# Performance work log

Measured on AMD Instinct MI355X. Metric: run time of the kernel, lower is better.

## Reference

```python
import jax, jax.numpy as jnp
import numpy as np

SHAPES = [(16, 32, 32), (8, 16, 16), (4, 8, 8), (2, 4, 4)]  # (D,H,W) per level
B, DM, M, LV, P, NL, DFF = 2, 256, 8, 4, 4, 2, 1024
DH = DM // M
LEN = sum(d * h * w for d, h, w in SHAPES)
EPS = 1e-5


def setup_inputs() -> dict:
    key = jax.random.key(0)
    ks = iter(jax.random.split(key, 64))
    inp = {}
    for i, (d_, h_, w_) in enumerate(SHAPES):
        inp[f"src{i}"] = jax.random.normal(next(ks), (B, DM, d_, h_, w_), jnp.float32)
        inp[f"pos{i}"] = jax.random.normal(next(ks), (B, DM, d_, h_, w_), jnp.float32) * 0.1
    inp["level_embed"] = jax.random.normal(next(ks), (LV, DM), jnp.float32)
    s = 1.0 / np.sqrt(DM)
    inp["W_off"] = jax.random.normal(next(ks), (NL, DM, M * LV * P * 3), jnp.float32) * 0.02
    inp["b_off"] = jax.random.normal(next(ks), (NL, M * LV * P * 3), jnp.float32) * 0.2
    inp["W_attn"] = jax.random.normal(next(ks), (NL, DM, M * LV * P), jnp.float32) * s
    inp["b_attn"] = jnp.zeros((NL, M * LV * P), jnp.float32)
    inp["W_val"] = jax.random.normal(next(ks), (NL, DM, DM), jnp.float32) * s
    inp["b_val"] = jnp.zeros((NL, DM), jnp.float32)
    inp["W_out"] = jax.random.normal(next(ks), (NL, DM, DM), jnp.float32) * s
    inp["b_out"] = jnp.zeros((NL, DM), jnp.float32)
    inp["ln1_g"] = jnp.ones((NL, DM), jnp.float32)
    inp["ln1_b"] = jnp.zeros((NL, DM), jnp.float32)
    inp["W_ff1"] = jax.random.normal(next(ks), (NL, DM, DFF), jnp.float32) * s
    inp["b_ff1"] = jnp.zeros((NL, DFF), jnp.float32)
    inp["W_ff2"] = jax.random.normal(next(ks), (NL, DFF, DM), jnp.float32) * (1.0 / np.sqrt(DFF))
    inp["b_ff2"] = jnp.zeros((NL, DM), jnp.float32)
    inp["ln2_g"] = jnp.ones((NL, DM), jnp.float32)
    inp["ln2_b"] = jnp.zeros((NL, DM), jnp.float32)
    return inp


def _layer_norm(x, g, b):
    mu = jnp.mean(x, -1, keepdims=True)
    var = jnp.mean(jnp.square(x - mu), -1, keepdims=True)
    return (x - mu) * jax.lax.rsqrt(var + EPS) * g + b


def _trilinear_sample(value_bm, loc, D_, H_, W_):
    """value_bm: [B, M, D*H*W, DH]; loc: [B, Lq, M, P, 3] normalized in [0,1].
    grid_sample(align_corners=False, padding=zeros) semantics: comp0->W, comp1->H, comp2->D."""
    x = loc[..., 0] * W_ - 0.5
    y = loc[..., 1] * H_ - 0.5
    z = loc[..., 2] * D_ - 0.5
    x0, y0, z0 = jnp.floor(x), jnp.floor(y), jnp.floor(z)
    fx, fy, fz = x - x0, y - y0, z - z0
    x0i, y0i, z0i = x0.astype(jnp.int32), y0.astype(jnp.int32), z0.astype(jnp.int32)
    Bq, Lq = loc.shape[0], loc.shape[1]
    out = jnp.zeros((Bq, M, Lq * P, DH), value_bm.dtype)
    for dz in (0, 1):
        for dy in (0, 1):
            for dx in (0, 1):
                xi, yi, zi = x0i + dx, y0i + dy, z0i + dz
                w = ((fx if dx else 1.0 - fx) * (fy if dy else 1.0 - fy) * (fz if dz else 1.0 - fz))
                valid = ((xi >= 0) & (xi < W_) & (yi >= 0) & (yi < H_) & (zi >= 0) & (zi < D_))
                idx = (jnp.clip(zi, 0, D_ - 1) * H_ + jnp.clip(yi, 0, H_ - 1)) * W_ + jnp.clip(xi, 0, W_ - 1)
                idx_bm = jnp.transpose(idx, (0, 2, 1, 3)).reshape(Bq, M, Lq * P)  # [B,M,Lq*P]
                v = jnp.take_along_axis(value_bm, idx_bm[..., None], axis=2)  # [B,M,Lq*P,DH]
                wv = jnp.transpose(w * valid, (0, 2, 1, 3)).reshape(Bq, M, Lq * P, 1)
                out = out + v * wv
    return out.reshape(Bq, M, Lq, P, DH)


def _forward(src0, src1, src2, src3, pos0, pos1, pos2, pos3, level_embed,
             W_off, b_off, W_attn, b_attn, W_val, b_val, W_out, b_out,
             ln1_g, ln1_b, W_ff1, b_ff1, W_ff2, b_ff2, ln2_g, ln2_b):
    srcs = [src0, src1, src2, src3]
    poss = [pos0, pos1, pos2, pos3]
    sizes = [d * h * w for d, h, w in SHAPES]
    # flatten [B,C,D,H,W] -> [B,DHW,C]
    src = jnp.concatenate([s.reshape(B, DM, -1).transpose(0, 2, 1) for s in srcs], axis=1)
    lvl_pos = jnp.concatenate(
        [p.reshape(B, DM, -1).transpose(0, 2, 1) + level_embed[l][None, None, :]
         for l, p in enumerate(poss)], axis=1)
    # reference points (valid_ratios == 1): component order (z/D, y/H, x/W) as in torch code
    refs = []
    for d_, h_, w_ in SHAPES:
        zz, yy, xx = jnp.meshgrid((jnp.arange(d_) + 0.5) / d_, (jnp.arange(h_) + 0.5) / h_,
                                  (jnp.arange(w_) + 0.5) / w_, indexing="ij")
        refs.append(jnp.stack([zz.ravel(), yy.ravel(), xx.ravel()], -1))
    ref = jnp.concatenate(refs, 0).astype(src.dtype)  # [LEN,3]
    normalizer = jnp.array([[w_, h_, d_] for d_, h_, w_ in SHAPES], src.dtype)  # [LV,3] = (W,H,D)

    offsets_splits = np.cumsum(sizes)[:-1]
    for l in range(NL):
        q = src + lvl_pos
        value = (src @ W_val[l] + b_val[l]).reshape(B, LEN, M, DH)
        off = (q @ W_off[l] + b_off[l]).reshape(B, LEN, M, LV, P, 3)
        attn = jax.nn.softmax((q @ W_attn[l] + b_attn[l]).reshape(B, LEN, M, LV * P), axis=-1)
        attn = attn.reshape(B, LEN, M, LV, P)
        loc = ref[None, :, None, None, None, :] + off / normalizer[None, None, None, :, None, :]
        value_levels = jnp.split(value, offsets_splits, axis=1)
        agg = jnp.zeros((B, LEN, M, DH), src.dtype)
        for lvl, (d_, h_, w_) in enumerate(SHAPES):
            value_bm = value_levels[lvl].transpose(0, 2, 1, 3)  # [B,M,Sl,DH]
            sampled = _trilinear_sample(value_bm, loc[:, :, :, lvl], d_, h_, w_)  # [B,M,LEN,P,DH]
            agg = agg + jnp.einsum("bmqpc,bqmp->bqmc", sampled, attn[:, :, :, lvl])
        out = agg.reshape(B, LEN, DM) @ W_out[l] + b_out[l]
        src = _layer_norm(src + out, ln1_g[l], ln1_b[l])
        ff = jax.nn.relu(src @ W_ff1[l] + b_ff1[l]) @ W_ff2[l] + b_ff2[l]
        src = _layer_norm(src + ff, ln2_g[l], ln2_b[l])
    return src


def reference(src0, src1, src2, src3, pos0, pos1, pos2, pos3, level_embed,
              W_off, b_off, W_attn, b_attn, W_val, b_val, W_out, b_out,
              ln1_g, ln1_b, W_ff1, b_ff1, W_ff2, b_ff2, ln2_g, ln2_b):
    return _forward(src0, src1, src2, src3, pos0, pos1, pos2, pos3, level_embed,
                    W_off, b_off, W_attn, b_attn, W_val, b_val, W_out, b_out,
                    ln1_g, ln1_b, W_ff1, b_ff1, W_ff2, b_ff2, ln2_g, ln2_b)
```

## Files before the change

### kernel.cpp

```cpp
#include <hip/hip_runtime.h>
#include <hip/hip_bf16.h>
#include <math.h>

typedef __attribute__((ext_vector_type(4))) float f32x4;
typedef __attribute__((ext_vector_type(8))) short bf16x8;

static constexpr int B_   = 2;
static constexpr int DM_  = 256;
static constexpr int NL_  = 2;
static constexpr int LEN_ = 18720;
static constexpr int NQ_  = 37440;
static constexpr int NQP_ = 37504;

__device__ __forceinline__ unsigned short f2bf(float x) {
    __hip_bfloat16 h = __float2bfloat16(x);
    return *reinterpret_cast<unsigned short*>(&h);
}

struct FlatArgs { const float* s[4]; const float* p[4]; };
__global__ __launch_bounds__(256) void k_flatten(FlatArgs a, const float* __restrict__ lemb,
                                                 float* __restrict__ src,
                                                 unsigned short* __restrict__ srcbf,
                                                 float* __restrict__ pos,
                                                 unsigned short* __restrict__ qbf) {
    int t = blockIdx.x, c = threadIdx.x;
    int l, rel;
    if (t < 32768)      { l = 0; rel = t; }
    else if (t < 36864) { l = 1; rel = t - 32768; }
    else if (t < 37376) { l = 2; rel = t - 36864; }
    else                { l = 3; rel = t - 37376; }
    const int SH[4] = {14, 11, 8, 5};
    const int OFF[4] = {0, 16384, 18432, 18688};
    int S = 1 << SH[l];
    int b = rel >> SH[l], s = rel & (S - 1);
    float sv = a.s[l][(size_t)(b * DM_ + c) * S + s];
    float pv = a.p[l][(size_t)(b * DM_ + c) * S + s] + lemb[l * DM_ + c];
    size_t row = (size_t)b * LEN_ + OFF[l] + s;
    src[row * DM_ + c] = sv;
    srcbf[row * DM_ + c] = f2bf(sv);
    pos[row * DM_ + c] = pv;
    qbf[row * DM_ + c] = f2bf(sv + pv);
}

struct WPEnt { const float* s; unsigned short* d; int K, N, start; };
struct WPArgs { WPEnt e[12]; };
__global__ __launch_bounds__(256) void k_wprep_all(WPArgs a) {
    __shared__ float t[32][33];
    int bidx = blockIdx.x;
    int i = 0;
#pragma unroll
    for (int j = 1; j < 12; ++j) if (bidx >= a.e[j].start) i = j;
    const float* W = a.e[i].s;
    unsigned short* Wt = a.e[i].d;
    int K = a.e[i].K, N = a.e[i].N;
    int ti = bidx - a.e[i].start;
    int tilesX = N >> 5;
    int bx = ti % tilesX, by = ti / tilesX;
    int n0 = bx * 32, k0 = by * 32;
    int tx = threadIdx.x & 31, ty = threadIdx.x >> 5;
#pragma unroll
    for (int q = 0; q < 4; ++q)
        t[ty + q * 8][tx] = W[(size_t)(k0 + ty + q * 8) * N + n0 + tx];
    __syncthreads();
#pragma unroll
    for (int q = 0; q < 4; ++q)
        Wt[(size_t)(n0 + ty + q * 8) * K + k0 + tx] = f2bf(t[tx][ty + q * 8]);
}

template<int K, int MODE>
__global__ __launch_bounds__(256) void k_gemm(const unsigned short* __restrict__ A,
                                              const unsigned short* __restrict__ Bt,
                                              const float* __restrict__ bias,
                                              const float* __restrict__ bias2,
                                              int nsplit,
                                              float* __restrict__ C,
                                              unsigned short* __restrict__ Cbf,
                                              int N) {
    __shared__ unsigned short As[128 * 32];
    __shared__ unsigned short Bs[128 * 32];
    int tid = threadIdx.x;
    int w = tid >> 6, lane = tid & 63;
    int wr = w >> 1, wc = w & 1;
    int row0 = blockIdx.x * 128, col0 = blockIdx.y * 128;

    const unsigned short* gA = A + (size_t)(row0 + w * 32 + (lane >> 2)) * K + (lane & 3) * 8;
    const unsigned short* gB = Bt + (size_t)(col0 + w * 32 + (lane >> 2)) * K + (lane & 3) * 8;
    char* lA0 = (char*)As + w * 2048;
    char* lB0 = (char*)Bs + w * 2048;

    f32x4 acc[4][4];
#pragma unroll
    for (int m = 0; m < 4; ++m)
#pragma unroll
        for (int n = 0; n < 4; ++n) acc[m][n] = (f32x4){0.f, 0.f, 0.f, 0.f};

    int lr = lane & 15, lk = (lane >> 4) * 8;
    const unsigned short* pA = &As[(wr * 64 + lr) * 32 + lk];
    const unsigned short* pB = &Bs[(wc * 64 + lr) * 32 + lk];

    for (int kt = 0; kt < K; kt += 32) {
        __builtin_amdgcn_global_load_lds((const __attribute__((address_space(1))) void*)gA,
                                         (__attribute__((address_space(3))) void*)lA0, 16, 0, 0);
        __builtin_amdgcn_global_load_lds((const __attribute__((address_space(1))) void*)(gA + (size_t)16 * K),
                                         (__attribute__((address_space(3))) void*)(lA0 + 1024), 16, 0, 0);
        __builtin_amdgcn_global_load_lds((const __attribute__((address_space(1))) void*)gB,
                                         (__attribute__((address_space(3))) void*)lB0, 16, 0, 0);
        __builtin_amdgcn_global_load_lds((const __attribute__((address_space(1))) void*)(gB + (size_t)16 * K),
                                         (__attribute__((address_space(3))) void*)(lB0 + 1024), 16, 0, 0);
        gA += 32; gB += 32;
        __syncthreads();
        bf16x8 a[4], b[4];
#pragma unroll
        for (int m = 0; m < 4; ++m) a[m] = *(const bf16x8*)(pA + m * 16 * 32);
#pragma unroll
        for (int n = 0; n < 4; ++n) b[n] = *(const bf16x8*)(pB + n * 16 * 32);
#pragma unroll
        for (int m = 0; m < 4; ++m)
#pragma unroll
            for (int n = 0; n < 4; ++n)
                acc[m][n] = __builtin_amdgcn_mfma_f32_16x16x32_bf16(a[m], b[n], acc[m][n], 0, 0, 0);
        __syncthreads();
    }

    int fr = (lane >> 4) * 4, fc = lane & 15;
#pragma unroll
    for (int m = 0; m < 4; ++m) {
#pragma unroll
        for (int n = 0; n < 4; ++n) {
            int cc = col0 + wc * 64 + n * 16 + fc;
            float bv = (cc < nsplit) ? bias[cc] : bias2[cc - nsplit];
#pragma unroll
            for (int i = 0; i < 4; ++i) {
                int cr = row0 + wr * 64 + m * 16 + fr + i;
                float v = acc[m][n][i] + bv;
                if (MODE == 1) {
                    Cbf[(size_t)cr * N + cc] = f2bf(fmaxf(v, 0.f));
                } else if (MODE == 2) {
                    Cbf[(size_t)cr * N + cc] = f2bf(v);
                } else {
                    C[(size_t)cr * N + cc] = v;
                }
            }
        }
    }
}

__global__ __launch_bounds__(256) void k_sample(const float* __restrict__ oa,
                                                const unsigned short* __restrict__ vbf,
                                                unsigned short* __restrict__ aggbf) {
    int bid = blockIdx.x;
    int row = (bid & 7) * (NQ_ / 8) + (bid >> 3);
    int b = row / LEN_, qi = row - b * LEN_;
    __shared__ float sw[8][128];
    __shared__ int sidx[8][128];
    int tid = threadIdx.x;

    int lq, s;
    if (qi < 16384)      { lq = 0; s = qi; }
    else if (qi < 18432) { lq = 1; s = qi - 16384; }
    else if (qi < 18688) { lq = 2; s = qi - 18432; }
    else                 { lq = 3; s = qi - 18688; }
    const int dD[4] = {16, 8, 4, 2}, dH[4] = {32, 16, 8, 4}, dW[4] = {32, 16, 8, 4};
    const int loff[4] = {0, 16384, 18432, 18688};
    int Dq = dD[lq], Hq = dH[lq], Wq = dW[lq];
    int zq = s / (Hq * Wq);
    int rr = s - zq * (Hq * Wq);
    int yq = rr / Wq, xq = rr - (rr / Wq) * Wq;
    float ref0 = (zq + 0.5f) / Dq, ref1 = (yq + 0.5f) / Hq, ref2 = (xq + 0.5f) / Wq;

    if (tid < 128) {
        int m = tid >> 4, l = (tid >> 2) & 3;
        float e = oa[(size_t)row * 512 + 384 + tid];
        float mx = e;
#pragma unroll
        for (int o = 1; o < 16; o <<= 1) mx = fmaxf(mx, __shfl_xor(mx, o, 16));
        float ex = expf(e - mx);
        float sm = ex;
#pragma unroll
        for (int o = 1; o < 16; o <<= 1) sm += __shfl_xor(sm, o, 16);
        float aw = ex / sm;

        const int D_ = dD[l], H_ = dH[l], W_ = dW[l];
        float o0 = oa[(size_t)row * 512 + tid * 3 + 0];
        float o1 = oa[(size_t)row * 512 + tid * 3 + 1];
        float o2 = oa[(size_t)row * 512 + tid * 3 + 2];
        float x = (ref0 + o0 / W_) * W_ - 0.5f;
        float y = (ref1 + o1 / H_) * H_ - 0.5f;
        float z = (ref2 + o2 / D_) * D_ - 0.5f;
        float xf = floorf(x), yf = floorf(y), zf = floorf(z);
        float fx = x - xf, fy = y - yf, fz = z - zf;
        int x0 = (int)xf, y0 = (int)yf, z0 = (int)zf;
        int vbase = (b * LEN_ + loff[l]) * DM_ + m * 32;
#pragma unroll
        for (int dz = 0; dz < 2; ++dz)
#pragma unroll
            for (int dy = 0; dy < 2; ++dy)
#pragma unroll
                for (int dx = 0; dx < 2; ++dx) {
                    int xi = x0 + dx, yi = y0 + dy, zi = z0 + dz;
                    float wgt = (dx ? fx : 1.f - fx) * (dy ? fy : 1.f - fy) * (dz ? fz : 1.f - fz);
                    bool valid = (xi >= 0) & (xi < W_) & (yi >= 0) & (yi < H_) &
                                 (zi >= 0) & (zi < D_);
                    int xc = min(max(xi, 0), W_ - 1);
                    int yc = min(max(yi, 0), H_ - 1);
                    int zc = min(max(zi, 0), D_ - 1);
                    int idx = (zc * H_ + yc) * W_ + xc;
                    int cr = (dz << 2) | (dy << 1) | dx;
                    sw[cr][tid] = valid ? aw * wgt : 0.f;
                    sidx[cr][tid] = vbase + idx * DM_;
                }
    }
    __syncthreads();

    int m = tid >> 5;
    int lane5 = tid & 31;
    int sub = lane5 >> 2, cg = lane5 & 3;
    float acc[8];
#pragma unroll
    for (int i = 0; i < 8; ++i) acc[i] = 0.f;
#pragma unroll
    for (int t = 0; t < 16; ++t) {
        int pair = sub * 16 + t;
        int tq = pair >> 3, cr = pair & 7;
        float wq = sw[cr][m * 16 + tq];
        int ofs = sidx[cr][m * 16 + tq];
        uint4 v = *(const uint4*)&vbf[ofs + cg * 8];
        float f0 = __uint_as_float(v.x << 16);
        float f1 = __uint_as_float(v.x & 0xffff0000u);
        float f2 = __uint_as_float(v.y << 16);
        float f3 = __uint_as_float(v.y & 0xffff0000u);
        float f4 = __uint_as_float(v.z << 16);
        float f5 = __uint_as_float(v.z & 0xffff0000u);
        float f6 = __uint_as_float(v.w << 16);
        float f7 = __uint_as_float(v.w & 0xffff0000u);
        acc[0] = fmaf(wq, f0, acc[0]);
        acc[1] = fmaf(wq, f1, acc[1]);
        acc[2] = fmaf(wq, f2, acc[2]);
        acc[3] = fmaf(wq, f3, acc[3]);
        acc[4] = fmaf(wq, f4, acc[4]);
        acc[5] = fmaf(wq, f5, acc[5]);
        acc[6] = fmaf(wq, f6, acc[6]);
        acc[7] = fmaf(wq, f7, acc[7]);
    }
#pragma unroll
    for (int i = 0; i < 8; ++i) {
        acc[i] += __shfl_xor(acc[i], 4, 64);
        acc[i] += __shfl_xor(acc[i], 8, 64);
        acc[i] += __shfl_xor(acc[i], 16, 64);
    }
    if (sub == 0) {
        uint4 o;
        o.x = ((unsigned)f2bf(acc[1]) << 16) | f2bf(acc[0]);
        o.y = ((unsigned)f2bf(acc[3]) << 16) | f2bf(acc[2]);
        o.z = ((unsigned)f2bf(acc[5]) << 16) | f2bf(acc[4]);
        o.w = ((unsigned)f2bf(acc[7]) << 16) | f2bf(acc[6]);
        *(uint4*)&aggbf[(size_t)row * DM_ + m * 32 + cg * 8] = o;
    }
}

__global__ __launch_bounds__(256) void k_add_ln(const float* __restrict__ X,
                                                const float* __restrict__ Rr,
                                                const float* __restrict__ g,
                                                const float* __restrict__ bb,
                                                float* __restrict__ O,
                                                unsigned short* __restrict__ Obf,
                                                const float* __restrict__ pos,
                                                unsigned short* __restrict__ qbf) {
    int wid = threadIdx.x >> 6, lane = threadIdx.x & 63;
    size_t row = (size_t)blockIdx.x * 4 + wid;
    float4 x = ((const float4*)&X[row * DM_])[lane];
    float4 r = ((const float4*)&Rr[row * DM_])[lane];
    float v[4] = {x.x + r.x, x.y + r.y, x.z + r.z, x.w + r.w};
    float sm = v[0] + v[1] + v[2] + v[3];
#pragma unroll
    for (int o = 32; o; o >>= 1) sm += __shfl_xor(sm, o, 64);
    float mu = sm * (1.f / 256.f);
    float q = 0.f;
#pragma unroll
    for (int i = 0; i < 4; ++i) { float d = v[i] - mu; q += d * d; }
#pragma unroll
    for (int o = 32; o; o >>= 1) q += __shfl_xor(q, o, 64);
    float inv = rsqrtf(q * (1.f / 256.f) + 1e-5f);
    int c0 = lane * 4;
    float4 gv = *(const float4*)&g[c0];
    float4 bv = *(const float4*)&bb[c0];
    float4 o4;
    o4.x = (v[0] - mu) * inv * gv.x + bv.x;
    o4.y = (v[1] - mu) * inv * gv.y + bv.y;
    o4.z = (v[2] - mu) * inv * gv.z + bv.z;
    o4.w = (v[3] - mu) * inv * gv.w + bv.w;
    ((float4*)&O[row * DM_])[lane] = o4;
    if (Obf) {
        ushort4 ob;
        ob.x = f2bf(o4.x); ob.y = f2bf(o4.y); ob.z = f2bf(o4.z); ob.w = f2bf(o4.w);
        ((ushort4*)&Obf[row * DM_])[lane] = ob;
    }
    if (qbf) {
        float4 pv = ((const float4*)&pos[row * DM_])[lane];
        ushort4 qb;
        qb.x = f2bf(o4.x + pv.x); qb.y = f2bf(o4.y + pv.y);
        qb.z = f2bf(o4.z + pv.z); qb.w = f2bf(o4.w + pv.w);
        ((ushort4*)&qbf[row * DM_])[lane] = qb;
    }
}

extern "C" void kernel_launch(void* const* d_in, const int* in_sizes, int n_in,
                              void* d_out, int out_size, void* d_ws, size_t ws_size,
                              hipStream_t stream) {
    const float* lemb  = (const float*)d_in[8];
    const float* W_off = (const float*)d_in[9];
    const float* bOff  = (const float*)d_in[10];
    const float* W_att = (const float*)d_in[11];
    const float* bAtt  = (const float*)d_in[12];
    const float* W_val = (const float*)d_in[13];
    const float* bVal  = (const float*)d_in[14];
    const float* W_out = (const float*)d_in[15];
    const float* bOut  = (const float*)d_in[16];
    const float* ln1g  = (const float*)d_in[17];
    const float* ln1b  = (const float*)d_in[18];
    const float* W_ff1 = (const float*)d_in[19];
    const float* bFf1  = (const float*)d_in[20];
    const float* W_ff2 = (const float*)d_in[21];
    const float* bFf2  = (const float*)d_in[22];
    const float* ln2g  = (const float*)d_in[23];
    const float* ln2b  = (const float*)d_in[24];

    char* ws = (char*)d_ws;
    const size_t NR = (size_t)NQP_ * 256;
    float* b_src = (float*)ws;
    float* b_pos = (float*)(ws + NR * 4);
    unsigned short* b_srcbf = (unsigned short*)(ws + NR * 8);
    unsigned short* b_qbf   = (unsigned short*)(ws + NR * 10);
    unsigned short* b_wt    = (unsigned short*)(ws + NR * 12);
    char* R = ws + NR * 12 + (size_t)2 * 786432 * 2;
    unsigned short* b_valbf = (unsigned short*)(R);
    float* b_oa             = (float*)(R + NR * 2);
    unsigned short* b_aggbf = (unsigned short*)(R + NR * 10);
    float* b_tmp            = (float*)(R);
    unsigned short* b_ffhbf = (unsigned short*)(R + NR * 4);
    float* b_tmp2           = (float*)(R);

    WPArgs wa;
    int start = 0;
    for (int l = 0; l < NL_; ++l) {
        unsigned short* wt = b_wt + (size_t)l * 786432;
        WPEnt ents[6] = {
            {W_val + (size_t)l * 65536,  wt + 0,      256, 256,  start},
            {W_off + (size_t)l * 98304,  wt + 65536,  256, 384,  start + 64},
            {W_att + (size_t)l * 32768,  wt + 163840, 256, 128,  start + 160},
            {W_out + (size_t)l * 65536,  wt + 196608, 256, 256,  start + 192},
            {W_ff1 + (size_t)l * 262144, wt + 262144, 256, 1024, start + 256},
            {W_ff2 + (size_t)l * 262144, wt + 524288, 1024, 256, start + 512},
        };
        for (int j = 0; j < 6; ++j) wa.e[l * 6 + j] = ents[j];
        start += 768;
    }
    k_wprep_all<<<dim3(1536), 256, 0, stream>>>(wa);

    FlatArgs fa;
    for (int i = 0; i < 4; ++i) {
        fa.s[i] = (const float*)d_in[2 * i];
        fa.p[i] = (const float*)d_in[2 * i + 1];
    }
    k_flatten<<<dim3(NQ_), 256, 0, stream>>>(fa, lemb, b_src, b_srcbf, b_pos, b_qbf);

    const int GR = NQP_ / 128;
    const int BIG = 1 << 30;
    for (int l = 0; l < NL_; ++l) {
        unsigned short* wt = b_wt + (size_t)l * 786432;
        k_gemm<256, 2><<<dim3(GR, 2), 256, 0, stream>>>(
            b_srcbf, wt + 0, bVal + l * 256, bVal + l * 256, BIG, nullptr, b_valbf, 256);
        k_gemm<256, 0><<<dim3(GR, 4), 256, 0, stream>>>(
            b_qbf, wt + 65536, bOff + l * 384, bAtt + l * 128, 384, b_oa, nullptr, 512);
        k_sample<<<dim3(NQ_), 256, 0, stream>>>(b_oa, b_valbf, b_aggbf);
        k_gemm<256, 0><<<dim3(GR, 2), 256, 0, stream>>>(
            b_aggbf, wt + 196608, bOut + l * 256, bOut + l * 256, BIG, b_tmp, nullptr, 256);
        k_add_ln<<<dim3(NQ_ / 4), 256, 0, stream>>>(b_src, b_tmp, ln1g + l * 256,
                                                    ln1b + l * 256, b_src, b_srcbf,
                                                    nullptr, nullptr);
        k_gemm<256, 1><<<dim3(GR, 8), 256, 0, stream>>>(
            b_srcbf, wt + 262144, bFf1 + l * 1024, bFf1 + l * 1024, BIG, nullptr, b_ffhbf, 1024);
        k_gemm<1024, 0><<<dim3(GR, 2), 256, 0, stream>>>(
            b_ffhbf, wt + 524288, bFf2 + l * 256, bFf2 + l * 256, BIG, b_tmp2, nullptr, 256);
        float* dst = (l == NL_ - 1) ? (float*)d_out : b_src;
        int last = (l == NL_ - 1);
        k_add_ln<<<dim3(NQ_ / 4), 256, 0, stream>>>(b_src, b_tmp2, ln2g + l * 256,
                                                    ln2b + l * 256, dst,
                                                    last ? nullptr : b_srcbf,
                                                    last ? nullptr : b_pos,
                                                    last ? nullptr : b_qbf);
    }
}
```

Measured before the change: 813.6 us.

## Fuse output and FFN2 GEMMs with residual add and LayerNorm

Adds a k_gemm_ln kernel in which each block computes a full 128x256 output tile, adds bias and the residual, and reduces row statistics across the two column-waves through shared memory. It then applies LayerNorm and writes the fp32, bf16 and query outputs directly. This removes the separate add_ln kernels and the fp32 round trip of the GEMM results through global memory. In exchange the grid has only 293 blocks with large per-thread accumulators, which lowers occupancy and parallelism, and variance is now computed in one pass as E[x^2]-mu^2.

```diff
diff --git a/kernel.cpp b/kernel.cpp
--- a/kernel.cpp
+++ b/kernel.cpp
@@ -145,6 +145,140 @@
     }
 }
 
+template<int K>
+__global__ __launch_bounds__(256) void k_gemm_ln(const unsigned short* __restrict__ A,
+                                                 const unsigned short* __restrict__ Bt,
+                                                 const float* __restrict__ bias,
+                                                 const float* __restrict__ X,
+                                                 const float* __restrict__ g,
+                                                 const float* __restrict__ bb,
+                                                 float* __restrict__ O,
+                                                 unsigned short* __restrict__ Obf,
+                                                 const float* __restrict__ pos,
+                                                 unsigned short* __restrict__ qbf) {
+    __shared__ unsigned short As[128 * 32];
+    __shared__ unsigned short Bs[256 * 32];
+    __shared__ float red[2][2][128];
+    int tid = threadIdx.x;
+    int w = tid >> 6, lane = tid & 63;
+    int wr = w >> 1, wc = w & 1;
+    int row0 = blockIdx.x * 128;
+
+    const unsigned short* gA = A + (size_t)(row0 + w * 32 + (lane >> 2)) * K + (lane & 3) * 8;
+    const unsigned short* gB = Bt + (size_t)(w * 64 + (lane >> 2)) * K + (lane & 3) * 8;
+    char* lA0 = (char*)As + w * 2048;
+    char* lB0 = (char*)Bs + w * 4096;
+
+    f32x4 acc[4][8];
+#pragma unroll
+    for (int m = 0; m < 4; ++m)
+#pragma unroll
+        for (int n = 0; n < 8; ++n) acc[m][n] = (f32x4){0.f, 0.f, 0.f, 0.f};
+
+    int lr = lane & 15, lk = (lane >> 4) * 8;
+    const unsigned short* pA = &As[(wr * 64 + lr) * 32 + lk];
+    const unsigned short* pB = &Bs[(wc * 128 + lr) * 32 + lk];
+
+    for (int kt = 0; kt < K; kt += 32) {
+        __builtin_amdgcn_global_load_lds((const __attribute__((address_space(1))) void*)gA,
+                                         (__attribute__((address_space(3))) void*)lA0, 16, 0, 0);
+        __builtin_amdgcn_global_load_lds((const __attribute__((address_space(1))) void*)(gA + (size_t)16 * K),
+                                         (__attribute__((address_space(3))) void*)(lA0 + 1024), 16, 0, 0);
+#pragma unroll
+        for (int c = 0; c < 4; ++c)
+            __builtin_amdgcn_global_load_lds(
+                (const __attribute__((address_space(1))) void*)(gB + (size_t)(c * 16) * K),
+                (__attribute__((address_space(3))) void*)(lB0 + c * 1024), 16, 0, 0);
+        gA += 32; gB += 32;
+        __syncthreads();
+        bf16x8 a[4], b[8];
+#pragma unroll
+        for (int m = 0; m < 4; ++m) a[m] = *(const bf16x8*)(pA + m * 16 * 32);
+#pragma unroll
+        for (int n = 0; n < 8; ++n) b[n] = *(const bf16x8*)(pB + n * 16 * 32);
+#pragma unroll
+        for (int m = 0; m < 4; ++m)
+#pragma unroll
+            for (int n = 0; n < 8; ++n)
+                acc[m][n] = __builtin_amdgcn_mfma_f32_16x16x32_bf16(a[m], b[n], acc[m][n], 0, 0, 0);
+        __syncthreads();
+    }
+
+    int fr = (lane >> 4) * 4, fc = lane & 15;
+    float biasv[8], gv[8], bv[8];
+#pragma unroll
+    for (int n = 0; n < 8; ++n) {
+        int c = wc * 128 + n * 16 + fc;
+        biasv[n] = bias[c]; gv[n] = g[c]; bv[n] = bb[c];
+    }
+    float s1[4][4], s2[4][4];
+#pragma unroll
+    for (int m = 0; m < 4; ++m)
+#pragma unroll
+        for (int i = 0; i < 4; ++i) { s1[m][i] = 0.f; s2[m][i] = 0.f; }
+#pragma unroll
+    for (int m = 0; m < 4; ++m) {
+#pragma unroll
+        for (int i = 0; i < 4; ++i) {
+            int row = row0 + wr * 64 + m * 16 + fr + i;
+            const float* xr = &X[(size_t)row * 256 + wc * 128 + fc];
+#pragma unroll
+            for (int n = 0; n < 8; ++n) {
+                float v = acc[m][n][i] + biasv[n] + xr[n * 16];
+                acc[m][n][i] = v;
+                s1[m][i] += v;
+                s2[m][i] = fmaf(v, v, s2[m][i]);
+            }
+        }
+    }
+#pragma unroll
+    for (int o = 1; o < 16; o <<= 1) {
+#pragma unroll
+        for (int m = 0; m < 4; ++m)
+#pragma unroll
+            for (int i = 0; i < 4; ++i) {
+                s1[m][i] += __shfl_xor(s1[m][i], o, 64);
+                s2[m][i] += __shfl_xor(s2[m][i], o, 64);
+            }
+    }
+    if (fc == 0) {
+#pragma unroll
+        for (int m = 0; m < 4; ++m)
+#pragma unroll
+            for (int i = 0; i < 4; ++i) {
+                int r = wr * 64 + m * 16 + fr + i;
+                red[wc][0][r] = s1[m][i];
+                red[wc][1][r] = s2[m][i];
+            }
+    }
+    __syncthreads();
+#pragma unroll
+    for (int m = 0; m < 4; ++m) {
+#pragma unroll
+        for (int i = 0; i < 4; ++i) {
+            int r = wr * 64 + m * 16 + fr + i;
+            int row = row0 + r;
+            if (row >= NQ_) continue;
+            float t1 = red[0][0][r] + red[1][0][r];
+            float t2 = red[0][1][r] + red[1][1][r];
+            float mu = t1 * (1.f / 256.f);
+            float inv = rsqrtf(t2 * (1.f / 256.f) - mu * mu + 1e-5f);
+            float* orow = &O[(size_t)row * 256 + wc * 128 + fc];
+            unsigned short* obrow = Obf ? &Obf[(size_t)row * 256 + wc * 128 + fc] : nullptr;
+#pragma unroll
+            for (int n = 0; n < 8; ++n) {
+                float y = (acc[m][n][i] - mu) * inv * gv[n] + bv[n];
+                orow[n * 16] = y;
+                if (Obf) obrow[n * 16] = f2bf(y);
+                if (qbf) {
+                    float pv = pos[(size_t)row * 256 + wc * 128 + n * 16 + fc];
+                    qbf[(size_t)row * 256 + wc * 128 + n * 16 + fc] = f2bf(y + pv);
+                }
+            }
+        }
+    }
+}
+
 __global__ __launch_bounds__(256) void k_sample(const float* __restrict__ oa,
                                                 const unsigned short* __restrict__ vbf,
                                                 unsigned short* __restrict__ aggbf) {
@@ -225,22 +359,14 @@
         float wq = sw[cr][m * 16 + tq];
         int ofs = sidx[cr][m * 16 + tq];
         uint4 v = *(const uint4*)&vbf[ofs + cg * 8];
-        float f0 = __uint_as_float(v.x << 16);
-        float f1 = __uint_as_float(v.x & 0xffff0000u);
-        float f2 = __uint_as_float(v.y << 16);
-        float f3 = __uint_as_float(v.y & 0xffff0000u);
-        float f4 = __uint_as_float(v.z << 16);
-        float f5 = __uint_as_float(v.z & 0xffff0000u);
-        float f6 = __uint_as_float(v.w << 16);
-        float f7 = __uint_as_float(v.w & 0xffff0000u);
-        acc[0] = fmaf(wq, f0, acc[0]);
-        acc[1] = fmaf(wq, f1, acc[1]);
-        acc[2] = fmaf(wq, f2, acc[2]);
-        acc[3] = fmaf(wq, f3, acc[3]);
-        acc[4] = fmaf(wq, f4, acc[4]);
-        acc[5] = fmaf(wq, f5, acc[5]);
-        acc[6] = fmaf(wq, f6, acc[6]);
-        acc[7] = fmaf(wq, f7, acc[7]);
+        acc[0] = fmaf(wq, __uint_as_float(v.x << 16), acc[0]);
+        acc[1] = fmaf(wq, __uint_as_float(v.x & 0xffff0000u), acc[1]);
+        acc[2] = fmaf(wq, __uint_as_float(v.y << 16), acc[2]);
+        acc[3] = fmaf(wq, __uint_as_float(v.y & 0xffff0000u), acc[3]);
+        acc[4] = fmaf(wq, __uint_as_float(v.z << 16), acc[4]);
+        acc[5] = fmaf(wq, __uint_as_float(v.z & 0xffff0000u), acc[5]);
+        acc[6] = fmaf(wq, __uint_as_float(v.w << 16), acc[6]);
+        acc[7] = fmaf(wq, __uint_as_float(v.w & 0xffff0000u), acc[7]);
     }
 #pragma unroll
     for (int i = 0; i < 8; ++i) {
@@ -255,52 +381,6 @@
         o.z = ((unsigned)f2bf(acc[5]) << 16) | f2bf(acc[4]);
         o.w = ((unsigned)f2bf(acc[7]) << 16) | f2bf(acc[6]);
         *(uint4*)&aggbf[(size_t)row * DM_ + m * 32 + cg * 8] = o;
-    }
-}
-
-__global__ __launch_bounds__(256) void k_add_ln(const float* __restrict__ X,
-                                                const float* __restrict__ Rr,
-                                                const float* __restrict__ g,
-                                                const float* __restrict__ bb,
-                                                float* __restrict__ O,
-                                                unsigned short* __restrict__ Obf,
-                                                const float* __restrict__ pos,
-                                                unsigned short* __restrict__ qbf) {
-    int wid = threadIdx.x >> 6, lane = threadIdx.x & 63;
-    size_t row = (size_t)blockIdx.x * 4 + wid;
-    float4 x = ((const float4*)&X[row * DM_])[lane];
-    float4 r = ((const float4*)&Rr[row * DM_])[lane];
-    float v[4] = {x.x + r.x, x.y + r.y, x.z + r.z, x.w + r.w};
-    float sm = v[0] + v[1] + v[2] + v[3];
-#pragma unroll
-    for (int o = 32; o; o >>= 1) sm += __shfl_xor(sm, o, 64);
-    float mu = sm * (1.f / 256.f);
-    float q = 0.f;
-#pragma unroll
-    for (int i = 0; i < 4; ++i) { float d = v[i] - mu; q += d * d; }
-#pragma unroll
-    for (int o = 32; o; o >>= 1) q += __shfl_xor(q, o, 64);
-    float inv = rsqrtf(q * (1.f / 256.f) + 1e-5f);
-    int c0 = lane * 4;
-    float4 gv = *(const float4*)&g[c0];
-    float4 bv = *(const float4*)&bb[c0];
-    float4 o4;
-    o4.x = (v[0] - mu) * inv * gv.x + bv.x;
-    o4.y = (v[1] - mu) * inv * gv.y + bv.y;
-    o4.z = (v[2] - mu) * inv * gv.z + bv.z;
-    o4.w = (v[3] - mu) * inv * gv.w + bv.w;
-    ((float4*)&O[row * DM_])[lane] = o4;
-    if (Obf) {
-        ushort4 ob;
-        ob.x = f2bf(o4.x); ob.y = f2bf(o4.y); ob.z = f2bf(o4.z); ob.w = f2bf(o4.w);
-        ((ushort4*)&Obf[row * DM_])[lane] = ob;
-    }
-    if (qbf) {
-        float4 pv = ((const float4*)&pos[row * DM_])[lane];
-        ushort4 qb;
-        qb.x = f2bf(o4.x + pv.x); qb.y = f2bf(o4.y + pv.y);
-        qb.z = f2bf(o4.z + pv.z); qb.w = f2bf(o4.w + pv.w);
-        ((ushort4*)&qbf[row * DM_])[lane] = qb;
     }
 }
 
@@ -336,9 +416,7 @@
     unsigned short* b_valbf = (unsigned short*)(R);
     float* b_oa             = (float*)(R + NR * 2);
     unsigned short* b_aggbf = (unsigned short*)(R + NR * 10);
-    float* b_tmp            = (float*)(R);
     unsigned short* b_ffhbf = (unsigned short*)(R + NR * 4);
-    float* b_tmp2           = (float*)(R);
 
     WPArgs wa;
     int start = 0;
@@ -368,26 +446,21 @@
     const int BIG = 1 << 30;
     for (int l = 0; l < NL_; ++l) {
         unsigned short* wt = b_wt + (size_t)l * 786432;
+        int last = (l == NL_ - 1);
         k_gemm<256, 2><<<dim3(GR, 2), 256, 0, stream>>>(
             b_srcbf, wt + 0, bVal + l * 256, bVal + l * 256, BIG, nullptr, b_valbf, 256);
         k_gemm<256, 0><<<dim3(GR, 4), 256, 0, stream>>>(
             b_qbf, wt + 65536, bOff + l * 384, bAtt + l * 128, 384, b_oa, nullptr, 512);
         k_sample<<<dim3(NQ_), 256, 0, stream>>>(b_oa, b_valbf, b_aggbf);
-        k_gemm<256, 0><<<dim3(GR, 2), 256, 0, stream>>>(
-            b_aggbf, wt + 196608, bOut + l * 256, bOut + l * 256, BIG, b_tmp, nullptr, 256);
-        k_add_ln<<<dim3(NQ_ / 4), 256, 0, stream>>>(b_src, b_tmp, ln1g + l * 256,
-                                                    ln1b + l * 256, b_src, b_srcbf,
-                                                    nullptr, nullptr);
+        k_gemm_ln<256><<<dim3(GR), 256, 0, stream>>>(
+            b_aggbf, wt + 196608, bOut + l * 256, b_src, ln1g + l * 256, ln1b + l * 256,
+            b_src, b_srcbf, nullptr, nullptr);
         k_gemm<256, 1><<<dim3(GR, 8), 256, 0, stream>>>(
             b_srcbf, wt + 262144, bFf1 + l * 1024, bFf1 + l * 1024, BIG, nullptr, b_ffhbf, 1024);
-        k_gemm<1024, 0><<<dim3(GR, 2), 256, 0, stream>>>(
-            b_ffhbf, wt + 524288, bFf2 + l * 256, bFf2 + l * 256, BIG, b_tmp2, nullptr, 256);
-        float* dst = (l == NL_ - 1) ? (float*)d_out : b_src;
-        int last = (l == NL_ - 1);
-        k_add_ln<<<dim3(NQ_ / 4), 256, 0, stream>>>(b_src, b_tmp2, ln2g + l * 256,
-                                                    ln2b + l * 256, dst,
-                                                    last ? nullptr : b_srcbf,
-                                                    last ? nullptr : b_pos,
-                                                    last ? nullptr : b_qbf);
-    }
-}
+        float* dst = last ? (float*)d_out : b_src;
+        k_gemm_ln<1024><<<dim3(GR), 256, 0, stream>>>(
+            b_ffhbf, wt + 524288, bFf2 + l * 256, b_src, ln2g + l * 256, ln2b + l * 256,
+            dst, last ? nullptr : b_srcbf,
+            last ? nullptr : b_pos, last ? nullptr : b_qbf);
+    }
+}
```

New measurement: 1.038 ms. 27.5% more time.
